# Optimization experiments

Hardware: AMD Instinct MI355X
Metric: run time of the kernel (lower is better)

Reference implementation:

```python
import jax, jax.numpy as jnp
import numpy as np

B, N, E, P, NH = 8, 1024, 768, 768, 12
HD = P // NH


def setup_inputs() -> dict:
    key = jax.random.key(0)
    ks = jax.random.split(key, 9)
    s = lambda k, sh: jax.random.normal(k, sh, dtype=jnp.float32) * 0.02
    return {
        "x": jax.random.normal(ks[0], (B, N, E), dtype=jnp.float32),
        "wq": s(ks[1], (E, P)), "bq": jnp.zeros((P,), jnp.float32),
        "wk": s(ks[2], (E, P)), "bk": jnp.zeros((P,), jnp.float32),
        "wv": s(ks[3], (E, P)), "bv": jnp.zeros((P,), jnp.float32),
        "wo": s(ks[4], (P, E)), "bo": jnp.zeros((E,), jnp.float32),
        "H": 32, "W": 32,
    }


def reference(x, wq, bq, wk, bk, wv, bv, wo, bo, H, W):
    b, n, _ = x.shape
    # QKV projections: [B,N,P] -> [B,NH,N,HD]
    def split_heads(t):
        return t.reshape(b, n, NH, HD).transpose(0, 2, 1, 3)
    q = split_heads(x @ wq + bq)
    k = split_heads(x @ wk + bk)
    v = split_heads(x @ wv + bv)
    # NOTE: original module applies NO 1/sqrt(head_dim) scaling.
    logits = jnp.einsum("bhqd,bhkd->bhqk", q, k)  # [B,NH,N,N]
    attn = jax.nn.softmax(logits, axis=-1)
    ctx = jnp.einsum("bhqk,bhkd->bhqd", attn, v)  # [B,NH,N,HD]
    ctx = ctx.transpose(0, 2, 1, 3).reshape(b, n, P)
    return ctx @ wo + bo
```

## Files before the change

### kernel.cpp

```cpp
#include <hip/hip_runtime.h>
#include <hip/hip_bf16.h>
#include <math.h>

#define B_   8
#define N_   1024
#define E_   768
#define P_   768
#define NH_  12
#define HD_  64
#define L2E  1.44269504088896340736f

typedef __attribute__((ext_vector_type(8))) short short8;
typedef __attribute__((ext_vector_type(4))) float f32x4;

__device__ inline void async16(void* lds, const void* g) {
    __builtin_amdgcn_global_load_lds(
        (const __attribute__((address_space(1))) void*)g,
        (__attribute__((address_space(3))) void*)lds, 16, 0, 0);
}

__device__ inline unsigned pkbf(float a, float b) {
    union { float f; unsigned u; } ua, ub;
    ua.f = a; ub.f = b;
    return __builtin_amdgcn_perm(ub.u, ua.u, 0x07060302u);
}

__global__ __launch_bounds__(256) void cvt_x(const float* __restrict__ x,
                                             __hip_bfloat16* __restrict__ xb, int n4) {
    int i = blockIdx.x * blockDim.x + threadIdx.x;
    const int stride = gridDim.x * blockDim.x;
    for (; i < n4; i += stride) {
        float4 f = ((const float4*)x)[i];
        union { __hip_bfloat16 h[4]; uint2 u; } pk;
        pk.h[0] = __float2bfloat16(f.x);
        pk.h[1] = __float2bfloat16(f.y);
        pk.h[2] = __float2bfloat16(f.z);
        pk.h[3] = __float2bfloat16(f.w);
        ((uint2*)xb)[i] = pk.u;
    }
}

__global__ __launch_bounds__(256) void cvt_tw(
    const float* __restrict__ W0, const float* __restrict__ W1,
    const float* __restrict__ W2, const float* __restrict__ W3,
    __hip_bfloat16* __restrict__ T0, __hip_bfloat16* __restrict__ T1,
    __hip_bfloat16* __restrict__ T2, __hip_bfloat16* __restrict__ T3) {
    const int z = blockIdx.z;
    const float* W = (z == 0) ? W0 : (z == 1) ? W1 : (z == 2) ? W2 : W3;
    __hip_bfloat16* T = (z == 0) ? T0 : (z == 1) ? T1 : (z == 2) ? T2 : T3;
    __shared__ float t[32][33];
    const int tx = threadIdx.x & 31, ty = threadIdx.x >> 5;
    const int n0 = blockIdx.x * 32, k0 = blockIdx.y * 32;
#pragma unroll
    for (int rr = 0; rr < 4; ++rr)
        t[ty + rr * 8][tx] = W[(k0 + ty + rr * 8) * 768 + n0 + tx];
    __syncthreads();
#pragma unroll
    for (int rr = 0; rr < 4; ++rr)
        T[(long)(n0 + ty + rr * 8) * 768 + k0 + tx] = __float2bfloat16(t[tx][ty + rr * 8]);
}

template <int NC>
__global__ __launch_bounds__(256) void gemm_core(
    const __hip_bfloat16* __restrict__ A0, const __hip_bfloat16* __restrict__ A1,
    const __hip_bfloat16* __restrict__ A2,
    const __hip_bfloat16* __restrict__ B01, const __hip_bfloat16* __restrict__ B2,
    const float* __restrict__ b0, const float* __restrict__ b1,
    const float* __restrict__ b2,
    void* __restrict__ C0, void* __restrict__ C1, void* __restrict__ C2,
    int fused) {
    constexpr int ABUF = 8192;
    constexpr int BBUF = NC * 64;
    constexpr int JT = NC / 32;
    __shared__ char As[3 * ABUF];
    __shared__ char Bs[3 * BBUF];

    const __hip_bfloat16* Arows;
    const __hip_bfloat16* Brows;
    const float* bias;
    void* Cout;
    int mode, rb, cb;
    if (fused) {
        const int xcd = blockIdx.x & 7, t = blockIdx.x >> 3;
        const int g = t % 18, yhi = t / 18;
        const int y = yhi * 8 + xcd;
        if (g < 12) {
            mode = 2;
            const int z = g / 6;
            rb = (g % 6) * 128; cb = y * 128;
            Arows = z ? A1 : A0; Brows = B01; bias = z ? b1 : b0; Cout = z ? C1 : C0;
        } else {
            mode = 1;
            rb = y * 128; cb = (g - 12) * 128;
            Arows = A2; Brows = B2; bias = b2; Cout = C2;
        }
    } else {
        mode = 3;
        const int xcd = blockIdx.x & 7, t = blockIdx.x >> 3;
        const int e = t % 6, thi = t / 6;
        const int tc = thi * 8 + xcd;
        rb = e * 128; cb = tc * NC;
        Arows = A0; Brows = B01; bias = b0; Cout = C0;
    }

    const int tid = threadIdx.x;
    const int lane = tid & 63;
    const int w = tid >> 6;
    const int l15 = lane & 15;
    const int quad = lane >> 4;
    const int mh = (w >> 1) * 64;
    const int nh = (w & 1) * (NC / 2);

    f32x4 acc[4][JT];
#pragma unroll
    for (int i = 0; i < 4; ++i)
#pragma unroll
        for (int j = 0; j < JT; ++j) acc[i][j] = (f32x4){0.f, 0.f, 0.f, 0.f};

    const int c1 = tid + 256;
    const int ar0 = tid >> 2, alc0 = (tid & 3) ^ ((ar0 >> 1) & 3);
    const int ar1 = c1 >> 2,  alc1 = (c1 & 3) ^ ((ar1 >> 1) & 3);
    const __hip_bfloat16* gA0 = Arows + (long)(rb + ar0) * 768 + alc0 * 8;
    const __hip_bfloat16* gA1 = Arows + (long)(rb + ar1) * 768 + alc1 * 8;
    const __hip_bfloat16* gB0 = Brows + (long)(cb + ar0) * 768 + alc0 * 8;
    const __hip_bfloat16* gB1 = (NC == 128) ? (Brows + (long)(cb + ar1) * 768 + alc1 * 8) : nullptr;

    async16(As + tid * 16, gA0);
    async16(As + c1 * 16, gA1);
    async16(Bs + tid * 16, gB0);
    if (NC == 128) async16(Bs + c1 * 16, gB1);
    async16(As + ABUF + tid * 16, gA0 + 32);
    async16(As + ABUF + c1 * 16, gA1 + 32);
    async16(Bs + BBUF + tid * 16, gB0 + 32);
    if (NC == 128) async16(Bs + BBUF + c1 * 16, gB1 + 32);

    for (int it = 0; it < 24; ++it) {
        const int bi = it % 3;
        const int boA = bi * ABUF;
        const int boB = bi * BBUF;
        if (it < 23) {
            if (NC == 128) asm volatile("s_waitcnt vmcnt(4)" ::: "memory");
            else           asm volatile("s_waitcnt vmcnt(3)" ::: "memory");
        } else {
            asm volatile("s_waitcnt vmcnt(0)" ::: "memory");
        }
        __builtin_amdgcn_s_barrier();
        asm volatile("" ::: "memory");
        if (it + 2 < 24) {
            const int pb = (it + 2) % 3;
            const int k2 = (it + 2) * 32;
            async16(As + pb * ABUF + tid * 16, gA0 + k2);
            async16(As + pb * ABUF + c1 * 16, gA1 + k2);
            async16(Bs + pb * BBUF + tid * 16, gB0 + k2);
            if (NC == 128) async16(Bs + pb * BBUF + c1 * 16, gB1 + k2);
        }

        short8 a[4], b[JT];
#pragma unroll
        for (int i = 0; i < 4; ++i) {
            const int row = mh + i * 16 + l15;
            a[i] = *(const short8*)(As + boA + row * 64 + (quad ^ ((row >> 1) & 3)) * 16);
        }
#pragma unroll
        for (int j = 0; j < JT; ++j) {
            const int row = nh + j * 16 + l15;
            b[j] = *(const short8*)(Bs + boB + row * 64 + (quad ^ ((row >> 1) & 3)) * 16);
        }
        __builtin_amdgcn_s_setprio(1);
#pragma unroll
        for (int i = 0; i < 4; ++i)
#pragma unroll
            for (int j = 0; j < JT; ++j)
                acc[i][j] = __builtin_amdgcn_mfma_f32_16x16x32_bf16(a[i], b[j], acc[i][j], 0, 0, 0);
        __builtin_amdgcn_s_setprio(0);
    }

    if (mode == 2) {
        __hip_bfloat16* O = (__hip_bfloat16*)Cout;
#pragma unroll
        for (int j = 0; j < JT; ++j) {
            const int n = cb + nh + j * 16 + l15;
            const int bb = n >> 10, nn = n & 1023;
#pragma unroll
            for (int i = 0; i < 4; ++i) {
                const int p0 = rb + mh + i * 16 + quad * 4;
                const int h = p0 >> 6, d0 = p0 & 63;
                const float4 bv = *(const float4*)(bias + p0);
                union { __hip_bfloat16 h4[4]; unsigned long long u; } pk;
                pk.h4[0] = __float2bfloat16(acc[i][j][0] + bv.x);
                pk.h4[1] = __float2bfloat16(acc[i][j][1] + bv.y);
                pk.h4[2] = __float2bfloat16(acc[i][j][2] + bv.z);
                pk.h4[3] = __float2bfloat16(acc[i][j][3] + bv.w);
                *(unsigned long long*)(O + (((long)(bb * NH_ + h)) * N_ + nn) * HD_ + d0) = pk.u;
            }
        }
    } else if (mode == 1) {
        __hip_bfloat16* O = (__hip_bfloat16*)Cout;
#pragma unroll
        for (int j = 0; j < JT; ++j) {
            const int p = cb + nh + j * 16 + l15;
            const int h = p >> 6, d = p & 63;
            const float bv = bias[p];
#pragma unroll
            for (int i = 0; i < 4; ++i) {
                const int n0 = rb + mh + i * 16 + quad * 4;
                const int bb = n0 >> 10, nn = n0 & 1023;
                union { __hip_bfloat16 h4[4]; unsigned long long u; } pk;
#pragma unroll
                for (int r = 0; r < 4; ++r)
                    pk.h4[r] = __float2bfloat16(acc[i][j][r] + bv);
                *(unsigned long long*)(O + (((long)(bb * NH_ + h)) * HD_ + d) * N_ + nn) = pk.u;
            }
        }
    } else {
        float* O = (float*)Cout;
#pragma unroll
        for (int j = 0; j < JT; ++j) {
            const int n = cb + nh + j * 16 + l15;
#pragma unroll
            for (int i = 0; i < 4; ++i) {
                const int e0 = rb + mh + i * 16 + quad * 4;
                const float4 bv = *(const float4*)(bias + e0);
                float4 vo;
                vo.x = acc[i][j][0] + bv.x;
                vo.y = acc[i][j][1] + bv.y;
                vo.z = acc[i][j][2] + bv.z;
                vo.w = acc[i][j][3] + bv.w;
                *(float4*)(O + (long)n * 768 + e0) = vo;
            }
        }
    }
}

__global__ __launch_bounds__(256, 3) void attn_mfma(
    const __hip_bfloat16* __restrict__ Q, const __hip_bfloat16* __restrict__ K,
    const __hip_bfloat16* __restrict__ Vt, __hip_bfloat16* __restrict__ ctx) {
    __shared__ __hip_bfloat16 Ks[3 * 64 * 64];
    __shared__ __hip_bfloat16 Vs[3 * 64 * 64];

    const int tid = threadIdx.x;
    const int lane = tid & 63, w = tid >> 6;
    const int l15 = lane & 15, quad = lane >> 4;
    const int y3 = l15 & 7;

    const int bx = blockIdx.x;
    const int rr_ = bx & 7, t_ = bx >> 3;
    const int qb = t_ & 7, hi_ = t_ >> 3;
    const int H = hi_ * 8 + rr_;
    const int bz = H / 12, hy = H - bz * 12;
    const long headOff = (long)H * (N_ * HD_);
    const int qBase = qb * 128;

    short8 qf[2][2];
#pragma unroll
    for (int i = 0; i < 2; ++i)
#pragma unroll
        for (int ks = 0; ks < 2; ++ks)
            qf[i][ks] = *(const short8*)(Q + headOff +
                (long)(qBase + w * 32 + i * 16 + l15) * HD_ + ks * 32 + quad * 8);
    asm volatile("" :: "v"(qf[0][0]), "v"(qf[0][1]), "v"(qf[1][0]), "v"(qf[1][1]));

    f32x4 o[4][2];
#pragma unroll
    for (int mt = 0; mt < 4; ++mt)
#pragma unroll
        for (int i = 0; i < 2; ++i) o[mt][i] = (f32x4){0.f, 0.f, 0.f, 0.f};
    f32x4 ol[2];
    ol[0] = (f32x4){0.f, 0.f, 0.f, 0.f};
    ol[1] = (f32x4){0.f, 0.f, 0.f, 0.f};
    const short8 onesv = (short8){0x3F80, 0x3F80, 0x3F80, 0x3F80,
                                  0x3F80, 0x3F80, 0x3F80, 0x3F80};

    const int p0 = tid, p1 = tid + 256;
    const int r0 = p0 >> 3, lc0 = (p0 & 7) ^ (r0 & 7);
    const int r1 = p1 >> 3, lc1 = (p1 & 7) ^ (r1 & 7);
    const __hip_bfloat16* gK0 = K + headOff + r0 * HD_ + lc0 * 8;
    const __hip_bfloat16* gK1 = K + headOff + r1 * HD_ + lc1 * 8;
    const __hip_bfloat16* gV0 = Vt + headOff + r0 * N_ + lc0 * 8;
    const __hip_bfloat16* gV1 = Vt + headOff + r1 * N_ + lc1 * 8;
    const int q0 = p0 * 16, q1 = p1 * 16;

    async16((char*)Ks + q0, gK0);
    async16((char*)Ks + q1, gK1);
    async16((char*)Vs + q0, gV0);
    async16((char*)Vs + q1, gV1);
    async16((char*)Ks + 8192 + q0, gK0 + (long)64 * HD_);
    async16((char*)Ks + 8192 + q1, gK1 + (long)64 * HD_);
    async16((char*)Vs + 8192 + q0, gV0 + 64);
    async16((char*)Vs + 8192 + q1, gV1 + 64);

    for (int it = 0; it < 16; ++it) {
        const int bo = (it % 3) * 8192;
        if (it < 15) asm volatile("s_waitcnt vmcnt(4)" ::: "memory");
        else         asm volatile("s_waitcnt vmcnt(0)" ::: "memory");
        __builtin_amdgcn_s_barrier();
        asm volatile("" ::: "memory");
        if (it + 2 < 16) {
            const int po = ((it + 2) % 3) * 8192;
            const long j1 = (long)(it + 2) * 64;
            async16((char*)Ks + po + q0, gK0 + j1 * HD_);
            async16((char*)Ks + po + q1, gK1 + j1 * HD_);
            async16((char*)Vs + po + q0, gV0 + j1);
            async16((char*)Vs + po + q1, gV1 + j1);
        }

        f32x4 sT[4][2];
#pragma unroll
        for (int n = 0; n < 4; ++n)
#pragma unroll
            for (int i = 0; i < 2; ++i) sT[n][i] = (f32x4){0.f, 0.f, 0.f, 0.f};
#pragma unroll
        for (int ks = 0; ks < 2; ++ks) {
            short8 kf[4];
#pragma unroll
            for (int n = 0; n < 4; ++n)
                kf[n] = *(const short8*)((char*)Ks + bo +
                    ((n * 16 + l15) * 64 + (((ks * 4 + quad) ^ y3) * 8)) * 2);
            __builtin_amdgcn_s_setprio(1);
#pragma unroll
            for (int n = 0; n < 4; ++n)
#pragma unroll
                for (int i = 0; i < 2; ++i)
                    sT[n][i] = __builtin_amdgcn_mfma_f32_16x16x32_bf16(kf[n], qf[i][ks], sT[n][i], 0, 0, 0);
            __builtin_amdgcn_s_setprio(0);
        }

        short8 pf[2][2];
#pragma unroll
        for (int i = 0; i < 2; ++i) {
            float pv[4][4];
#pragma unroll
            for (int n = 0; n < 4; ++n)
#pragma unroll
                for (int r = 0; r < 4; ++r)
                    pv[n][r] = __expf(sT[n][i][r] - 16.635532333438686f);
            union { unsigned u[4]; short8 v; } pk0, pk1;
            pk0.u[0] = pkbf(pv[0][0], pv[0][1]);
            pk0.u[1] = pkbf(pv[0][2], pv[0][3]);
            pk0.u[2] = pkbf(pv[1][0], pv[1][1]);
            pk0.u[3] = pkbf(pv[1][2], pv[1][3]);
            pk1.u[0] = pkbf(pv[2][0], pv[2][1]);
            pk1.u[1] = pkbf(pv[2][2], pv[2][3]);
            pk1.u[2] = pkbf(pv[3][0], pv[3][1]);
            pk1.u[3] = pkbf(pv[3][2], pv[3][3]);
            pf[i][0] = pk0.v;
            pf[i][1] = pk1.v;
        }

#pragma unroll
        for (int g = 0; g < 2; ++g) {
#pragma unroll
            for (int mt = 0; mt < 4; ++mt) {
                const int row = mt * 16 + l15;
                union { short s4[2][4]; short8 v; } vb;
#pragma unroll
                for (int h = 0; h < 2; ++h) {
                    const int chunk = g * 4 + h * 2 + (quad >> 1);
                    *(long*)vb.s4[h] = *(const long*)((char*)Vs + bo +
                        (row * 64 + ((chunk ^ y3) * 8 + (quad & 1) * 4)) * 2);
                }
                __builtin_amdgcn_s_setprio(1);
#pragma unroll
                for (int i = 0; i < 2; ++i)
                    o[mt][i] = __builtin_amdgcn_mfma_f32_16x16x32_bf16(vb.v, pf[i][g], o[mt][i], 0, 0, 0);
                __builtin_amdgcn_s_setprio(0);
            }
#pragma unroll
            for (int i = 0; i < 2; ++i)
                ol[i] = __builtin_amdgcn_mfma_f32_16x16x32_bf16(onesv, pf[i][g], ol[i], 0, 0, 0);
        }
    }

#pragma unroll
    for (int i = 0; i < 2; ++i) {
        const float inv = 1.0f / ol[i][0];
        const int q = qBase + w * 32 + i * 16 + l15;
        __hip_bfloat16* op = ctx + ((long)(bz * N_ + q)) * P_ + hy * HD_;
#pragma unroll
        for (int mt = 0; mt < 4; ++mt) {
            union { __hip_bfloat16 h[4]; unsigned long long u; } pk;
#pragma unroll
            for (int r = 0; r < 4; ++r)
                pk.h[r] = __float2bfloat16(o[mt][i][r] * inv);
            *(unsigned long long*)(op + mt * 16 + quad * 4) = pk.u;
        }
    }
}

extern "C" void kernel_launch(void* const* d_in, const int* in_sizes, int n_in,
                              void* d_out, int out_size, void* d_ws, size_t ws_size,
                              hipStream_t stream) {
    const float* x  = (const float*)d_in[0];
    const float* wq = (const float*)d_in[1];
    const float* bq = (const float*)d_in[2];
    const float* wk = (const float*)d_in[3];
    const float* bk = (const float*)d_in[4];
    const float* wv = (const float*)d_in[5];
    const float* bv = (const float*)d_in[6];
    const float* wo = (const float*)d_in[7];
    const float* bo = (const float*)d_in[8];
    float* out = (float*)d_out;

    char* p = (char*)d_ws;
    const long XB = (long)B_ * N_ * E_ * 2;
    const long WB = (long)E_ * P_ * 2;
    const long HB = (long)B_ * NH_ * N_ * HD_ * 2;
    __hip_bfloat16* xb  = (__hip_bfloat16*)p; p += XB;
    __hip_bfloat16* wqt = (__hip_bfloat16*)p; p += WB;
    __hip_bfloat16* wkt = (__hip_bfloat16*)p; p += WB;
    __hip_bfloat16* wvt = (__hip_bfloat16*)p; p += WB;
    __hip_bfloat16* wot = (__hip_bfloat16*)p; p += WB;
    __hip_bfloat16* qh  = (__hip_bfloat16*)p; p += HB;
    __hip_bfloat16* kh  = (__hip_bfloat16*)p; p += HB;
    __hip_bfloat16* vth = (__hip_bfloat16*)p; p += HB;
    __hip_bfloat16* ctxb = (__hip_bfloat16*)p; p += HB;

    cvt_x<<<2048, 256, 0, stream>>>(x, xb, (B_ * N_ * E_) / 4);
    cvt_tw<<<dim3(24, 24, 4), 256, 0, stream>>>(wq, wk, wv, wo, wqt, wkt, wvt, wot);

    gemm_core<128><<<dim3(1152), 256, 0, stream>>>(
        wqt, wkt, xb, xb, wvt, bq, bk, bv, qh, kh, vth, 1);

    attn_mfma<<<dim3(768), 256, 0, stream>>>(qh, kh, vth, ctxb);

    gemm_core<64><<<dim3(768), 256, 0, stream>>>(
        wot, wot, wot, ctxb, ctxb, bo, bo, bo, out, out, out, 0);
}
```

Measured before the change: 220.9 us.

## Hand-schedule LDS reads with inline asm and widen output GEMM tile

Replaces the compiler-generated LDS fragment loads in the GEMM and attention kernels with inline ds_read_b128/ds_read_b64 that use precomputed base addresses and immediate offsets. Explicit lgkmcnt waits and sched_barriers are added so K and V fragment loads are issued early and overlap with MFMA work. The output projection switches to the 128-column GEMM tile with half as many blocks. The manual waitcnt scheduling is fragile, and the larger output tile lowers the block count and occupancy.

```diff
diff --git a/kernel.cpp b/kernel.cpp
--- a/kernel.cpp
+++ b/kernel.cpp
@@ -17,6 +17,10 @@
     __builtin_amdgcn_global_load_lds(
         (const __attribute__((address_space(1))) void*)g,
         (__attribute__((address_space(3))) void*)lds, 16, 0, 0);
+}
+
+__device__ inline unsigned lds_addr(const void* p) {
+    return (unsigned)(unsigned long long)(__attribute__((address_space(3))) const char*)p;
 }
 
 __device__ inline unsigned pkbf(float a, float b) {
@@ -125,6 +129,9 @@
     const __hip_bfloat16* gB0 = Brows + (long)(cb + ar0) * 768 + alc0 * 8;
     const __hip_bfloat16* gB1 = (NC == 128) ? (Brows + (long)(cb + ar1) * 768 + alc1 * 8) : nullptr;
 
+    const unsigned aBase0 = lds_addr(As) + (mh + l15) * 64 + ((quad ^ ((l15 >> 1) & 3)) << 4);
+    const unsigned bBase0 = lds_addr(Bs) + (nh + l15) * 64 + ((quad ^ ((l15 >> 1) & 3)) << 4);
+
     async16(As + tid * 16, gA0);
     async16(As + c1 * 16, gA1);
     async16(Bs + tid * 16, gB0);
@@ -155,17 +162,17 @@
             if (NC == 128) async16(Bs + pb * BBUF + c1 * 16, gB1 + k2);
         }
 
+        const unsigned aB = aBase0 + boA;
+        const unsigned bB = bBase0 + boB;
         short8 a[4], b[JT];
 #pragma unroll
-        for (int i = 0; i < 4; ++i) {
-            const int row = mh + i * 16 + l15;
-            a[i] = *(const short8*)(As + boA + row * 64 + (quad ^ ((row >> 1) & 3)) * 16);
-        }
-#pragma unroll
-        for (int j = 0; j < JT; ++j) {
-            const int row = nh + j * 16 + l15;
-            b[j] = *(const short8*)(Bs + boB + row * 64 + (quad ^ ((row >> 1) & 3)) * 16);
-        }
+        for (int i = 0; i < 4; ++i)
+            asm volatile("ds_read_b128 %0, %1 offset:%2" : "=v"(a[i]) : "v"(aB), "i"(i * 1024));
+#pragma unroll
+        for (int j = 0; j < JT; ++j)
+            asm volatile("ds_read_b128 %0, %1 offset:%2" : "=v"(b[j]) : "v"(bB), "i"(j * 1024));
+        asm volatile("s_waitcnt lgkmcnt(0)" ::: "memory");
+        __builtin_amdgcn_sched_barrier(0);
         __builtin_amdgcn_s_setprio(1);
 #pragma unroll
         for (int i = 0; i < 4; ++i)
@@ -279,6 +286,16 @@
     const __hip_bfloat16* gV0 = Vt + headOff + r0 * N_ + lc0 * 8;
     const __hip_bfloat16* gV1 = Vt + headOff + r1 * N_ + lc1 * 8;
     const int q0 = p0 * 16, q1 = p1 * 16;
+
+    const unsigned kfB0 = lds_addr(Ks) + (unsigned)(l15 * 128 + (((0 * 4 + quad) ^ y3) * 16));
+    const unsigned kfB1 = lds_addr(Ks) + (unsigned)(l15 * 128 + (((1 * 4 + quad) ^ y3) * 16));
+    unsigned vbB[2][2];
+#pragma unroll
+    for (int g = 0; g < 2; ++g)
+#pragma unroll
+        for (int h = 0; h < 2; ++h)
+            vbB[g][h] = lds_addr(Vs) + (unsigned)(l15 * 128 +
+                (((g * 4 + h * 2 + (quad >> 1)) ^ y3) * 16 + (quad & 1) * 8));
 
     async16((char*)Ks + q0, gK0);
     async16((char*)Ks + q1, gK1);
@@ -304,26 +321,46 @@
             async16((char*)Vs + po + q1, gV1 + j1);
         }
 
+        short8 kf[2][4];
+        {
+            const unsigned ka0 = kfB0 + bo, ka1 = kfB1 + bo;
+#pragma unroll
+            for (int n = 0; n < 4; ++n)
+                asm volatile("ds_read_b128 %0, %1 offset:%2" : "=v"(kf[0][n]) : "v"(ka0), "i"(n * 2048));
+#pragma unroll
+            for (int n = 0; n < 4; ++n)
+                asm volatile("ds_read_b128 %0, %1 offset:%2" : "=v"(kf[1][n]) : "v"(ka1), "i"(n * 2048));
+        }
         f32x4 sT[4][2];
 #pragma unroll
         for (int n = 0; n < 4; ++n)
 #pragma unroll
             for (int i = 0; i < 2; ++i) sT[n][i] = (f32x4){0.f, 0.f, 0.f, 0.f};
-#pragma unroll
-        for (int ks = 0; ks < 2; ++ks) {
-            short8 kf[4];
-#pragma unroll
-            for (int n = 0; n < 4; ++n)
-                kf[n] = *(const short8*)((char*)Ks + bo +
-                    ((n * 16 + l15) * 64 + (((ks * 4 + quad) ^ y3) * 8)) * 2);
-            __builtin_amdgcn_s_setprio(1);
-#pragma unroll
-            for (int n = 0; n < 4; ++n)
-#pragma unroll
-                for (int i = 0; i < 2; ++i)
-                    sT[n][i] = __builtin_amdgcn_mfma_f32_16x16x32_bf16(kf[n], qf[i][ks], sT[n][i], 0, 0, 0);
-            __builtin_amdgcn_s_setprio(0);
-        }
+        asm volatile("s_waitcnt lgkmcnt(4)" ::: "memory");
+        __builtin_amdgcn_sched_barrier(0);
+        __builtin_amdgcn_s_setprio(1);
+#pragma unroll
+        for (int n = 0; n < 4; ++n)
+#pragma unroll
+            for (int i = 0; i < 2; ++i)
+                sT[n][i] = __builtin_amdgcn_mfma_f32_16x16x32_bf16(kf[0][n], qf[i][0], sT[n][i], 0, 0, 0);
+        __builtin_amdgcn_s_setprio(0);
+        asm volatile("s_waitcnt lgkmcnt(0)" ::: "memory");
+        __builtin_amdgcn_sched_barrier(0);
+        __builtin_amdgcn_s_setprio(1);
+#pragma unroll
+        for (int n = 0; n < 4; ++n)
+#pragma unroll
+            for (int i = 0; i < 2; ++i)
+                sT[n][i] = __builtin_amdgcn_mfma_f32_16x16x32_bf16(kf[1][n], qf[i][1], sT[n][i], 0, 0, 0);
+        __builtin_amdgcn_s_setprio(0);
+
+        long v0[4][2];
+#pragma unroll
+        for (int mt = 0; mt < 4; ++mt)
+#pragma unroll
+            for (int h = 0; h < 2; ++h)
+                asm volatile("ds_read_b64 %0, %1 offset:%2" : "=v"(v0[mt][h]) : "v"(vbB[0][h] + bo), "i"(mt * 2048));
 
         short8 pf[2][2];
 #pragma unroll
@@ -347,28 +384,43 @@
             pf[i][1] = pk1.v;
         }
 
-#pragma unroll
-        for (int g = 0; g < 2; ++g) {
-#pragma unroll
-            for (int mt = 0; mt < 4; ++mt) {
-                const int row = mt * 16 + l15;
-                union { short s4[2][4]; short8 v; } vb;
-#pragma unroll
-                for (int h = 0; h < 2; ++h) {
-                    const int chunk = g * 4 + h * 2 + (quad >> 1);
-                    *(long*)vb.s4[h] = *(const long*)((char*)Vs + bo +
-                        (row * 64 + ((chunk ^ y3) * 8 + (quad & 1) * 4)) * 2);
-                }
-                __builtin_amdgcn_s_setprio(1);
-#pragma unroll
-                for (int i = 0; i < 2; ++i)
-                    o[mt][i] = __builtin_amdgcn_mfma_f32_16x16x32_bf16(vb.v, pf[i][g], o[mt][i], 0, 0, 0);
-                __builtin_amdgcn_s_setprio(0);
-            }
+        asm volatile("s_waitcnt lgkmcnt(0)" ::: "memory");
+        __builtin_amdgcn_sched_barrier(0);
+        __builtin_amdgcn_s_setprio(1);
+#pragma unroll
+        for (int mt = 0; mt < 4; ++mt) {
+            union { long l[2]; short8 v; } vb;
+            vb.l[0] = v0[mt][0]; vb.l[1] = v0[mt][1];
 #pragma unroll
             for (int i = 0; i < 2; ++i)
-                ol[i] = __builtin_amdgcn_mfma_f32_16x16x32_bf16(onesv, pf[i][g], ol[i], 0, 0, 0);
-        }
+                o[mt][i] = __builtin_amdgcn_mfma_f32_16x16x32_bf16(vb.v, pf[i][0], o[mt][i], 0, 0, 0);
+        }
+#pragma unroll
+        for (int i = 0; i < 2; ++i)
+            ol[i] = __builtin_amdgcn_mfma_f32_16x16x32_bf16(onesv, pf[i][0], ol[i], 0, 0, 0);
+        __builtin_amdgcn_s_setprio(0);
+
+        long v1[4][2];
+#pragma unroll
+        for (int mt = 0; mt < 4; ++mt)
+#pragma unroll
+            for (int h = 0; h < 2; ++h)
+                asm volatile("ds_read_b64 %0, %1 offset:%2" : "=v"(v1[mt][h]) : "v"(vbB[1][h] + bo), "i"(mt * 2048));
+        asm volatile("s_waitcnt lgkmcnt(0)" ::: "memory");
+        __builtin_amdgcn_sched_barrier(0);
+        __builtin_amdgcn_s_setprio(1);
+#pragma unroll
+        for (int mt = 0; mt < 4; ++mt) {
+            union { long l[2]; short8 v; } vb;
+            vb.l[0] = v1[mt][0]; vb.l[1] = v1[mt][1];
+#pragma unroll
+            for (int i = 0; i < 2; ++i)
+                o[mt][i] = __builtin_amdgcn_mfma_f32_16x16x32_bf16(vb.v, pf[i][1], o[mt][i], 0, 0, 0);
+        }
+#pragma unroll
+        for (int i = 0; i < 2; ++i)
+            ol[i] = __builtin_amdgcn_mfma_f32_16x16x32_bf16(onesv, pf[i][1], ol[i], 0, 0, 0);
+        __builtin_amdgcn_s_setprio(0);
     }
 
 #pragma unroll
@@ -423,6 +475,6 @@
 
     attn_mfma<<<dim3(768), 256, 0, stream>>>(qh, kh, vth, ctxb);
 
-    gemm_core<64><<<dim3(768), 256, 0, stream>>>(
+    gemm_core<128><<<dim3(384), 256, 0, stream>>>(
         wot, wot, wot, ctxb, ctxb, bo, bo, bo, out, out, out, 0);
 }
```

Result: faster. 203.4 us (-7.9%).
